# Kernel tuning notes

Measured on AMD Instinct MI355X. Metric: run time of the kernel, lower is better.

## Reference

```python
import jax, jax.numpy as jnp
import numpy as np

B, C, E, L = 128, 128, 10, 16  # atoms, channels, elements, num_ell (lmax=3)
K3_0, K2_0, K1_0 = 23, 4, 1    # num_params per correlation order, 0e output
K3_1, K2_1, K1_1 = 33, 6, 1    # num_params per correlation order, 1o output (num_equiv=3)


def setup_inputs() -> dict:
    key = jax.random.key(0)
    ks = jax.random.split(key, 16)
    inp = {
        'x': jax.random.normal(ks[0], (B, C, L), jnp.float32),
        'y': jax.random.uniform(ks[1], (B, E), jnp.float32),
        # generalized CG (U) buffers -- random dense stand-ins with faithful shapes
        'U1_0e': jax.random.normal(ks[2], (L, K1_0), jnp.float32),
        'U2_0e': jax.random.normal(ks[3], (L, L, K2_0), jnp.float32),
        'U3_0e': jax.random.normal(ks[4], (L, L, L, K3_0), jnp.float32),
        'U1_1o': jax.random.normal(ks[5], (3, L, K1_1), jnp.float32),
        'U2_1o': jax.random.normal(ks[6], (3, L, L, K2_1), jnp.float32),
        'U3_1o': jax.random.normal(ks[7], (3, L, L, L, K3_1), jnp.float32),
        # per-element weights, init randn/num_params as in torch
        'w1_0e': jax.random.normal(ks[8], (E, K1_0, C), jnp.float32) / K1_0,
        'w2_0e': jax.random.normal(ks[9], (E, K2_0, C), jnp.float32) / K2_0,
        'w3_0e': jax.random.normal(ks[10], (E, K3_0, C), jnp.float32) / K3_0,
        'w1_1o': jax.random.normal(ks[11], (E, K1_1, C), jnp.float32) / K1_1,
        'w2_1o': jax.random.normal(ks[12], (E, K2_1, C), jnp.float32) / K2_1,
        'w3_1o': jax.random.normal(ks[13], (E, K3_1, C), jnp.float32) / K3_1,
    }
    return inp


def _contract_0e(x, y, U1, U2, U3, w1, w2, w3):
    # main: 'wxik,ekc,bci,be->bcwx' (explicit path to control peak memory)
    wy3 = jnp.einsum('ekc,be->bkc', w3, y)              # [B,K3,C]
    t = jnp.einsum('wxik,bkc->bcwxi', U3, wy3)          # [B,C,L,L,L]
    out = jnp.einsum('bcwxi,bci->bcwx', t, x)           # [B,C,L,L]
    # order 2: weighting 'wxk,ekc,be->bcwx', features 'bcwi,bci->bcw'
    c2 = jnp.einsum('wxk,ekc,be->bcwx', U2, w2, y)
    out = jnp.einsum('bcwi,bci->bcw', c2 + out, x)
    # order 1: weighting 'wk,ekc,be->bcw', features 'bci,bci->bc'
    c1 = jnp.einsum('wk,ekc,be->bcw', U1, w1, y)
    out = jnp.einsum('bci,bci->bc', c1 + out, x)
    return out  # [B, C]


def _contract_1o(x, y, U1, U2, U3, w1, w2, w3):
    # main: 'wxvik,ekc,bci,be->bcwxv'  (w = equivariance dim of size 3)
    wy3 = jnp.einsum('ekc,be->bkc', w3, y)              # [B,K3,C]
    t = jnp.einsum('wxvik,bkc->bcwxvi', U3, wy3)        # [B,C,3,L,L,L]
    out = jnp.einsum('bcwxvi,bci->bcwxv', t, x)         # [B,C,3,L,L]
    # order 2: 'wxvk,ekc,be->bcwxv' ; features 'bcwxi,bci->bcwx'
    c2 = jnp.einsum('wxvk,ekc,be->bcwxv', U2, w2, y)
    out = jnp.einsum('bcwxi,bci->bcwx', c2 + out, x)
    # order 1: 'wxk,ekc,be->bcwx' ; features 'bcwi,bci->bcw'
    c1 = jnp.einsum('wxk,ekc,be->bcwx', U1, w1, y)
    out = jnp.einsum('bcwi,bci->bcw', c1 + out, x)
    return out.reshape(out.shape[0], -1)  # [B, 3*C]


def reference(x, y, U1_0e, U2_0e, U3_0e, U1_1o, U2_1o, U3_1o,
              w1_0e, w2_0e, w3_0e, w1_1o, w2_1o, w3_1o):
    out0 = _contract_0e(x, y, U1_0e, U2_0e, U3_0e, w1_0e, w2_0e, w3_0e)
    out1 = _contract_1o(x, y, U1_1o, U2_1o, U3_1o, w1_1o, w2_1o, w3_1o)
    return jnp.concatenate([out0, out1], axis=-1)  # [B, C + 3*C]
```

## Files before the change

### kernel.cpp

```cpp
#include <hip/hip_runtime.h>


typedef float  f32x4  __attribute__((ext_vector_type(4)));
typedef short  short8 __attribute__((ext_vector_type(8)));

namespace {
constexpr int EE  = 10;
constexpr int B1W = 552;
constexpr int B0W = 392;
constexpr int Z31 = 0;
constexpr int Z21 = 33;
constexpr int Z11 = 39;
constexpr int Z30 = 40;
constexpr int Z20 = 63;
constexpr int Z10 = 67;
constexpr int NZ  = 68;
}

__device__ __forceinline__ unsigned cvtpk(float lo, float hi) {
  unsigned r;
  asm("v_cvt_pk_bf16_f32 %0, %1, %2" : "=v"(r) : "v"(lo), "v"(hi));
  return r;
}

__device__ __forceinline__ short8 pack8(float f0, float f1, float f2, float f3,
                                        float f4, float f5, float f6, float f7) {
  union { short8 s; unsigned u[4]; } r;
  r.u[0] = cvtpk(f0, f1);
  r.u[1] = cvtpk(f2, f3);
  r.u[2] = cvtpk(f4, f5);
  r.u[3] = cvtpk(f6, f7);
  return r.s;
}

__global__ __launch_bounds__(512, 2) void symcon_mfma(
    const float* __restrict__ x,
    const float* __restrict__ y,
    const float* __restrict__ U1_0e,
    const float* __restrict__ U2_0e,
    const float* __restrict__ U3_0e,
    const float* __restrict__ U1_1o,
    const float* __restrict__ U2_1o,
    const float* __restrict__ U3_1o,
    const float* __restrict__ w1_0e, const float* __restrict__ w2_0e,
    const float* __restrict__ w3_0e, const float* __restrict__ w1_1o,
    const float* __restrict__ w2_1o, const float* __restrict__ w3_1o,
    float* __restrict__ out)
{
  __shared__ float x_lds[16][64];
  __shared__ float zbuf[NZ][64];
  __shared__ unsigned short B1buf[64][B1W];
  __shared__ unsigned short B0buf[64][B0W];
  __shared__ float red[8][64];

  const int tid   = threadIdx.x;
  const int blk   = blockIdx.x;
  const int pair0 = blk * 64;
  const int b     = blk >> 1;

  for (int t = tid; t < 16 * 64; t += 512) {
    const int i = t >> 6, n = t & 63;
    x_lds[i][n] = x[(size_t)(pair0 + n) * 16 + i];
  }
  for (int t = tid; t < NZ * 64; t += 512) {
    const int n  = t & 63;
    const int zi = t >> 6;
    const int c  = ((blk & 1) << 6) + n;
    const float* yb = y + b * EE;
    const float* wsrc; int stride;
    if      (zi < Z21) { wsrc = w3_1o + (zi      ) * 128 + c; stride = 33 * 128; }
    else if (zi < Z11) { wsrc = w2_1o + (zi - Z21) * 128 + c; stride =  6 * 128; }
    else if (zi < Z30) { wsrc = w1_1o +                    c; stride =  1 * 128; }
    else if (zi < Z20) { wsrc = w3_0e + (zi - Z30) * 128 + c; stride = 23 * 128; }
    else if (zi < Z10) { wsrc = w2_0e + (zi - Z20) * 128 + c; stride =  4 * 128; }
    else               { wsrc = w1_0e +                    c; stride =  1 * 128; }
    float a = 0.f;
    #pragma unroll
    for (int e = 0; e < EE; ++e) a += wsrc[e * stride] * yb[e];
    zbuf[zi][n] = a;
  }
  __syncthreads();

  auto b1valf = [&](int kap, int p) -> float {
    if (kap < 528) { int i = kap / 33, kk = kap - i * 33; return x_lds[i][p] * zbuf[Z31 + kk][p]; }
    if (kap < 534) return zbuf[Z21 + (kap - 528)][p];
    return 0.f;
  };
  auto b0valf = [&](int kap, int p) -> float {
    if (kap < 368) { int i = kap / 23, kk = kap - i * 23; return x_lds[i][p] * zbuf[Z30 + kk][p]; }
    if (kap < 372) return zbuf[Z20 + (kap - 368)][p];
    return 0.f;
  };
  #pragma unroll 1
  for (int idx = tid; idx < 272 * 64; idx += 512) {
    const int p = idx & 63, cp = idx >> 6;
    const int k0 = cp * 2;
    *(unsigned*)&B1buf[p][k0] = cvtpk(b1valf(k0, p), b1valf(k0 + 1, p));
  }
  #pragma unroll 1
  for (int idx = tid; idx < 192 * 64; idx += 512) {
    const int p = idx & 63, cp = idx >> 6;
    const int k0 = cp * 2;
    *(unsigned*)&B0buf[p][k0] = cvtpk(b0valf(k0, p), b0valf(k0 + 1, p));
  }
  __syncthreads();

  const int lane  = tid & 63;
  const int wv    = tid >> 6;
  const bool is1o = (wv < 6);
  const int q00   = (wv & 1) * 128;
  const int mbase = (is1o ? wv : (wv - 6)) * 128;
  const int lrow  = lane & 15;
  const int lgr   = lane >> 4;

  f32x4 acc[8][4] = {};

  if (is1o) {
    const float* __restrict__ U3r[8];
    #pragma unroll
    for (int mf = 0; mf < 8; ++mf)
      U3r[mf] = U3_1o + (size_t)(mbase + mf * 16 + lrow) * 528 + lgr * 8;
    #pragma unroll 2
    for (int t = 0; t < 16; ++t) {
      short8 af[8];
      #pragma unroll
      for (int mf = 0; mf < 8; ++mf) {
        f32x4 a  = *(const f32x4*)(U3r[mf] + t * 32);
        f32x4 bq = *(const f32x4*)(U3r[mf] + t * 32 + 4);
        af[mf] = pack8(a[0], a[1], a[2], a[3], bq[0], bq[1], bq[2], bq[3]);
      }
      short8 bfr[4];
      #pragma unroll
      for (int nf = 0; nf < 4; ++nf)
        bfr[nf] = *(const short8*)&B1buf[nf * 16 + lrow][t * 32 + lgr * 8];
      #pragma unroll
      for (int mf = 0; mf < 8; ++mf)
        #pragma unroll
        for (int nf = 0; nf < 4; ++nf)
          acc[mf][nf] = __builtin_amdgcn_mfma_f32_16x16x32_bf16(af[mf], bfr[nf], acc[mf][nf], 0, 0, 0);
    }
    {
      short8 af[8];
      #pragma unroll
      for (int mf = 0; mf < 8; ++mf) {
        const int row = mbase + mf * 16 + lrow;
        if (lgr < 2) {
          const float* p = U3_1o + (size_t)row * 528 + 512 + lgr * 8;
          f32x4 a = *(const f32x4*)p; f32x4 bq = *(const f32x4*)(p + 4);
          af[mf] = pack8(a[0], a[1], a[2], a[3], bq[0], bq[1], bq[2], bq[3]);
        } else if (lgr == 2) {
          const float* p = U2_1o + row * 6;
          af[mf] = pack8(p[0], p[1], p[2], p[3], p[4], p[5], 0.f, 0.f);
        } else {
          af[mf] = short8{0, 0, 0, 0, 0, 0, 0, 0};
        }
      }
      short8 bfr[4];
      #pragma unroll
      for (int nf = 0; nf < 4; ++nf)
        bfr[nf] = *(const short8*)&B1buf[nf * 16 + lrow][512 + lgr * 8];
      #pragma unroll
      for (int mf = 0; mf < 8; ++mf)
        #pragma unroll
        for (int nf = 0; nf < 4; ++nf)
          acc[mf][nf] = __builtin_amdgcn_mfma_f32_16x16x32_bf16(af[mf], bfr[nf], acc[mf][nf], 0, 0, 0);
    }
  } else {
    const float* __restrict__ U3r[8];
    #pragma unroll
    for (int mf = 0; mf < 8; ++mf)
      U3r[mf] = U3_0e + (size_t)(mbase + mf * 16 + lrow) * 368 + lgr * 8;
    #pragma unroll 2
    for (int t = 0; t < 11; ++t) {
      short8 af[8];
      #pragma unroll
      for (int mf = 0; mf < 8; ++mf) {
        f32x4 a  = *(const f32x4*)(U3r[mf] + t * 32);
        f32x4 bq = *(const f32x4*)(U3r[mf] + t * 32 + 4);
        af[mf] = pack8(a[0], a[1], a[2], a[3], bq[0], bq[1], bq[2], bq[3]);
      }
      short8 bfr[4];
      #pragma unroll
      for (int nf = 0; nf < 4; ++nf)
        bfr[nf] = *(const short8*)&B0buf[nf * 16 + lrow][t * 32 + lgr * 8];
      #pragma unroll
      for (int mf = 0; mf < 8; ++mf)
        #pragma unroll
        for (int nf = 0; nf < 4; ++nf)
          acc[mf][nf] = __builtin_amdgcn_mfma_f32_16x16x32_bf16(af[mf], bfr[nf], acc[mf][nf], 0, 0, 0);
    }
    {
      short8 af[8];
      #pragma unroll
      for (int mf = 0; mf < 8; ++mf) {
        const int row = mbase + mf * 16 + lrow;
        if (lgr < 2) {
          const float* p = U3_0e + (size_t)row * 368 + 352 + lgr * 8;
          f32x4 a = *(const f32x4*)p; f32x4 bq = *(const f32x4*)(p + 4);
          af[mf] = pack8(a[0], a[1], a[2], a[3], bq[0], bq[1], bq[2], bq[3]);
        } else if (lgr == 2) {
          const float* p = U2_0e + row * 4;
          af[mf] = pack8(p[0], p[1], p[2], p[3], 0.f, 0.f, 0.f, 0.f);
        } else {
          af[mf] = short8{0, 0, 0, 0, 0, 0, 0, 0};
        }
      }
      short8 bfr[4];
      #pragma unroll
      for (int nf = 0; nf < 4; ++nf)
        bfr[nf] = *(const short8*)&B0buf[nf * 16 + lrow][352 + lgr * 8];
      #pragma unroll
      for (int mf = 0; mf < 8; ++mf)
        #pragma unroll
        for (int nf = 0; nf < 4; ++nf)
          acc[mf][nf] = __builtin_amdgcn_mfma_f32_16x16x32_bf16(af[mf], bfr[nf], acc[mf][nf], 0, 0, 0);
    }
  }

  float s[4] = {0.f, 0.f, 0.f, 0.f};
  const int rg = lgr * 4;
  #pragma unroll
  for (int mf = 0; mf < 8; ++mf) {
    #pragma unroll
    for (int reg = 0; reg < 4; ++reg) {
      const int q  = q00 + mf * 16 + rg + reg;
      const int qa = q >> 4, qb = q & 15;
      #pragma unroll
      for (int nf = 0; nf < 4; ++nf) {
        const int p = nf * 16 + lrow;
        s[nf] += acc[mf][nf][reg] * (x_lds[qa][p] * x_lds[qb][p]);
      }
    }
  }
  #pragma unroll
  for (int nf = 0; nf < 4; ++nf) {
    s[nf] += __shfl_xor(s[nf], 16);
    s[nf] += __shfl_xor(s[nf], 32);
  }
  if (lane < 16) {
    #pragma unroll
    for (int nf = 0; nf < 4; ++nf) red[wv][nf * 16 + lane] = s[nf];
  }
  __syncthreads();

  if (tid < 256) {
    const int slot = tid >> 6;
    const int n    = tid & 63;
    const int cc   = ((blk & 1) << 6) + n;
    if (slot < 3) {
      float u1 = 0.f;
      #pragma unroll
      for (int xx = 0; xx < 16; ++xx) u1 += U1_1o[slot * 16 + xx] * x_lds[xx][n];
      out[(size_t)b * 512 + 128 + cc * 3 + slot] =
          red[2 * slot][n] + red[2 * slot + 1][n] + zbuf[Z11][n] * u1;
    } else {
      float u1 = 0.f;
      #pragma unroll
      for (int xx = 0; xx < 16; ++xx) u1 += U1_0e[xx] * x_lds[xx][n];
      out[(size_t)b * 512 + cc] =
          red[6][n] + red[7][n] + zbuf[Z10][n] * u1;
    }
  }
}

extern "C" void kernel_launch(void* const* d_in, const int* in_sizes, int n_in,
                              void* d_out, int out_size, void* d_ws, size_t ws_size,
                              hipStream_t stream) {
  const float* x     = (const float*)d_in[0];
  const float* y     = (const float*)d_in[1];
  const float* U1_0e = (const float*)d_in[2];
  const float* U2_0e = (const float*)d_in[3];
  const float* U3_0e = (const float*)d_in[4];
  const float* U1_1o = (const float*)d_in[5];
  const float* U2_1o = (const float*)d_in[6];
  const float* U3_1o = (const float*)d_in[7];
  const float* w1_0e = (const float*)d_in[8];
  const float* w2_0e = (const float*)d_in[9];
  const float* w3_0e = (const float*)d_in[10];
  const float* w1_1o = (const float*)d_in[11];
  const float* w2_1o = (const float*)d_in[12];
  const float* w3_1o = (const float*)d_in[13];
  (void)in_sizes; (void)n_in; (void)out_size; (void)d_ws; (void)ws_size;

  hipLaunchKernelGGL(symcon_mfma, dim3(256), dim3(512), 0, stream,
                     x, y, U1_0e, U2_0e, U3_0e, U1_1o, U2_1o, U3_1o,
                     w1_0e, w2_0e, w3_0e, w1_1o, w2_1o, w3_1o,
                     (float*)d_out);
}
```

Baseline: 54.94 us.

## Split 1o and 0e paths into separate blocks with smaller per-wave tiles

Each block previously handled both the 1o and 0e contractions for a 64-pair tile with 8 waves. The kernel now launches twice as many blocks of 12 waves. The first half computes only the 1o output, using 4 M-fragments per wave, and the second half computes only 0e, with 8 active waves of 2 fragments each. Shared memory is a union of the two layouts, which shrinks LDS per block. The intent is more parallelism, lower register pressure and better occupancy, at the cost of unbalanced block work and idle waves in the 0e blocks.

```diff
diff --git a/kernel.cpp b/kernel.cpp
--- a/kernel.cpp
+++ b/kernel.cpp
@@ -5,16 +5,21 @@
 typedef short  short8 __attribute__((ext_vector_type(8)));
 
 namespace {
-constexpr int EE  = 10;
-constexpr int B1W = 552;
-constexpr int B0W = 392;
-constexpr int Z31 = 0;
-constexpr int Z21 = 33;
-constexpr int Z11 = 39;
-constexpr int Z30 = 40;
-constexpr int Z20 = 63;
-constexpr int Z10 = 67;
-constexpr int NZ  = 68;
+constexpr int EE = 10;
+
+struct Sh1 {
+  unsigned short B1[64][552];
+  float x[16][64];
+  float z[40][64];
+  float red[12][64];
+};
+struct Sh0 {
+  unsigned short B0[64][392];
+  float x[16][64];
+  float z[28][64];
+  float red[8][64];
+};
+union ShU { Sh1 o1; Sh0 o0; };
 }
 
 __device__ __forceinline__ unsigned cvtpk(float lo, float hi) {
@@ -33,7 +38,7 @@
   return r.s;
 }
 
-__global__ __launch_bounds__(512, 2) void symcon_mfma(
+__global__ __launch_bounds__(768) void symcon_mfma(
     const float* __restrict__ x,
     const float* __restrict__ y,
     const float* __restrict__ U1_0e,
@@ -47,84 +52,74 @@
     const float* __restrict__ w2_1o, const float* __restrict__ w3_1o,
     float* __restrict__ out)
 {
-  __shared__ float x_lds[16][64];
-  __shared__ float zbuf[NZ][64];
-  __shared__ unsigned short B1buf[64][B1W];
-  __shared__ unsigned short B0buf[64][B0W];
-  __shared__ float red[8][64];
+  __shared__ ShU sh;
 
   const int tid   = threadIdx.x;
   const int blk   = blockIdx.x;
-  const int pair0 = blk * 64;
-  const int b     = blk >> 1;
-
-  for (int t = tid; t < 16 * 64; t += 512) {
-    const int i = t >> 6, n = t & 63;
-    x_lds[i][n] = x[(size_t)(pair0 + n) * 16 + i];
-  }
-  for (int t = tid; t < NZ * 64; t += 512) {
-    const int n  = t & 63;
-    const int zi = t >> 6;
-    const int c  = ((blk & 1) << 6) + n;
-    const float* yb = y + b * EE;
-    const float* wsrc; int stride;
-    if      (zi < Z21) { wsrc = w3_1o + (zi      ) * 128 + c; stride = 33 * 128; }
-    else if (zi < Z11) { wsrc = w2_1o + (zi - Z21) * 128 + c; stride =  6 * 128; }
-    else if (zi < Z30) { wsrc = w1_1o +                    c; stride =  1 * 128; }
-    else if (zi < Z20) { wsrc = w3_0e + (zi - Z30) * 128 + c; stride = 23 * 128; }
-    else if (zi < Z10) { wsrc = w2_0e + (zi - Z20) * 128 + c; stride =  4 * 128; }
-    else               { wsrc = w1_0e +                    c; stride =  1 * 128; }
-    float a = 0.f;
-    #pragma unroll
-    for (int e = 0; e < EE; ++e) a += wsrc[e * stride] * yb[e];
-    zbuf[zi][n] = a;
-  }
-  __syncthreads();
-
-  auto b1valf = [&](int kap, int p) -> float {
-    if (kap < 528) { int i = kap / 33, kk = kap - i * 33; return x_lds[i][p] * zbuf[Z31 + kk][p]; }
-    if (kap < 534) return zbuf[Z21 + (kap - 528)][p];
-    return 0.f;
-  };
-  auto b0valf = [&](int kap, int p) -> float {
-    if (kap < 368) { int i = kap / 23, kk = kap - i * 23; return x_lds[i][p] * zbuf[Z30 + kk][p]; }
-    if (kap < 372) return zbuf[Z20 + (kap - 368)][p];
-    return 0.f;
-  };
-  #pragma unroll 1
-  for (int idx = tid; idx < 272 * 64; idx += 512) {
-    const int p = idx & 63, cp = idx >> 6;
-    const int k0 = cp * 2;
-    *(unsigned*)&B1buf[p][k0] = cvtpk(b1valf(k0, p), b1valf(k0 + 1, p));
-  }
-  #pragma unroll 1
-  for (int idx = tid; idx < 192 * 64; idx += 512) {
-    const int p = idx & 63, cp = idx >> 6;
-    const int k0 = cp * 2;
-    *(unsigned*)&B0buf[p][k0] = cvtpk(b0valf(k0, p), b0valf(k0 + 1, p));
-  }
-  __syncthreads();
-
+  const bool is1o = (blk < 256);
+  const int pblk  = is1o ? blk : blk - 256;
+  const int pair0 = pblk * 64;
+  const int b     = pblk >> 1;
   const int lane  = tid & 63;
   const int wv    = tid >> 6;
-  const bool is1o = (wv < 6);
-  const int q00   = (wv & 1) * 128;
-  const int mbase = (is1o ? wv : (wv - 6)) * 128;
   const int lrow  = lane & 15;
   const int lgr   = lane >> 4;
 
-  f32x4 acc[8][4] = {};
-
   if (is1o) {
-    const float* __restrict__ U3r[8];
+    for (int t = tid; t < 16 * 64; t += 768) {
+      const int i = t >> 6, n = t & 63;
+      sh.o1.x[i][n] = x[(size_t)(pair0 + n) * 16 + i];
+    }
+    for (int t = tid; t < 40 * 64; t += 768) {
+      const int n  = t & 63;
+      const int zi = t >> 6;
+      const int c  = ((pblk & 1) << 6) + n;
+      const float* yb = y + b * EE;
+      const float* wsrc; int stride;
+      if      (zi < 33) { wsrc = w3_1o + zi * 128 + c;        stride = 33 * 128; }
+      else if (zi < 39) { wsrc = w2_1o + (zi - 33) * 128 + c; stride =  6 * 128; }
+      else              { wsrc = w1_1o + c;                   stride =      128; }
+      float a = 0.f;
+      #pragma unroll
+      for (int e = 0; e < EE; ++e) a += wsrc[e * stride] * yb[e];
+      sh.o1.z[zi][n] = a;
+    }
+    __syncthreads();
+
+    #pragma unroll 1
+    for (int idx = tid; idx < 272 * 64; idx += 768) {
+      const int p = idx & 63, cp = idx >> 6;
+      const int k0 = cp * 2;
+      float v0, v1;
+      if (k0 < 528) {
+        const int i = k0 / 33, kk = k0 - i * 33;
+        v0 = sh.o1.x[i][p] * sh.o1.z[kk][p];
+        const int k1 = k0 + 1;
+        const int i1 = k1 / 33, kk1 = k1 - i1 * 33;
+        v1 = sh.o1.x[i1][p] * sh.o1.z[kk1][p];
+      } else if (k0 < 534) {
+        v0 = sh.o1.z[33 + (k0 - 528)][p];
+        v1 = (k0 + 1 < 534) ? sh.o1.z[33 + (k0 - 527)][p] : 0.f;
+      } else {
+        v0 = 0.f; v1 = 0.f;
+      }
+      *(unsigned*)&sh.o1.B1[p][k0] = cvtpk(v0, v1);
+    }
+    __syncthreads();
+
+    const int mbase = wv * 64;
+    const float* __restrict__ U3r[4];
     #pragma unroll
-    for (int mf = 0; mf < 8; ++mf)
+    for (int mf = 0; mf < 4; ++mf)
       U3r[mf] = U3_1o + (size_t)(mbase + mf * 16 + lrow) * 528 + lgr * 8;
+
+    f32x4 acc[4][4] = {};
+
     #pragma unroll 2
     for (int t = 0; t < 16; ++t) {
-      short8 af[8];
-      #pragma unroll
-      for (int mf = 0; mf < 8; ++mf) {
+      short8 af[4];
+      #pragma unroll
+      for (int mf = 0; mf < 4; ++mf) {
         f32x4 a  = *(const f32x4*)(U3r[mf] + t * 32);
         f32x4 bq = *(const f32x4*)(U3r[mf] + t * 32 + 4);
         af[mf] = pack8(a[0], a[1], a[2], a[3], bq[0], bq[1], bq[2], bq[3]);
@@ -132,17 +127,17 @@
       short8 bfr[4];
       #pragma unroll
       for (int nf = 0; nf < 4; ++nf)
-        bfr[nf] = *(const short8*)&B1buf[nf * 16 + lrow][t * 32 + lgr * 8];
-      #pragma unroll
-      for (int mf = 0; mf < 8; ++mf)
+        bfr[nf] = *(const short8*)&sh.o1.B1[nf * 16 + lrow][t * 32 + lgr * 8];
+      #pragma unroll
+      for (int mf = 0; mf < 4; ++mf)
         #pragma unroll
         for (int nf = 0; nf < 4; ++nf)
           acc[mf][nf] = __builtin_amdgcn_mfma_f32_16x16x32_bf16(af[mf], bfr[nf], acc[mf][nf], 0, 0, 0);
     }
     {
-      short8 af[8];
-      #pragma unroll
-      for (int mf = 0; mf < 8; ++mf) {
+      short8 af[4];
+      #pragma unroll
+      for (int mf = 0; mf < 4; ++mf) {
         const int row = mbase + mf * 16 + lrow;
         if (lgr < 2) {
           const float* p = U3_1o + (size_t)row * 528 + 512 + lgr * 8;
@@ -158,107 +153,185 @@
       short8 bfr[4];
       #pragma unroll
       for (int nf = 0; nf < 4; ++nf)
-        bfr[nf] = *(const short8*)&B1buf[nf * 16 + lrow][512 + lgr * 8];
-      #pragma unroll
-      for (int mf = 0; mf < 8; ++mf)
+        bfr[nf] = *(const short8*)&sh.o1.B1[nf * 16 + lrow][512 + lgr * 8];
+      #pragma unroll
+      for (int mf = 0; mf < 4; ++mf)
         #pragma unroll
         for (int nf = 0; nf < 4; ++nf)
           acc[mf][nf] = __builtin_amdgcn_mfma_f32_16x16x32_bf16(af[mf], bfr[nf], acc[mf][nf], 0, 0, 0);
     }
+
+    float s[4] = {0.f, 0.f, 0.f, 0.f};
+    const int rg = lgr * 4;
+    #pragma unroll
+    for (int mf = 0; mf < 4; ++mf) {
+      #pragma unroll
+      for (int reg = 0; reg < 4; ++reg) {
+        const int q  = (mbase + mf * 16 + rg + reg) & 255;
+        const int qa = q >> 4, qb = q & 15;
+        #pragma unroll
+        for (int nf = 0; nf < 4; ++nf) {
+          const int p = nf * 16 + lrow;
+          s[nf] += acc[mf][nf][reg] * (sh.o1.x[qa][p] * sh.o1.x[qb][p]);
+        }
+      }
+    }
+    #pragma unroll
+    for (int nf = 0; nf < 4; ++nf) {
+      s[nf] += __shfl_xor(s[nf], 16);
+      s[nf] += __shfl_xor(s[nf], 32);
+    }
+    if (lane < 16) {
+      #pragma unroll
+      for (int nf = 0; nf < 4; ++nf) sh.o1.red[wv][nf * 16 + lane] = s[nf];
+    }
+    __syncthreads();
+
+    if (tid < 192) {
+      const int slot = tid >> 6;
+      const int n    = tid & 63;
+      const int cc   = ((pblk & 1) << 6) + n;
+      float v = sh.o1.red[4 * slot][n] + sh.o1.red[4 * slot + 1][n]
+              + sh.o1.red[4 * slot + 2][n] + sh.o1.red[4 * slot + 3][n];
+      float u1 = 0.f;
+      #pragma unroll
+      for (int xx = 0; xx < 16; ++xx) u1 += U1_1o[slot * 16 + xx] * sh.o1.x[xx][n];
+      out[(size_t)b * 512 + 128 + cc * 3 + slot] = v + sh.o1.z[39][n] * u1;
+    }
   } else {
-    const float* __restrict__ U3r[8];
-    #pragma unroll
-    for (int mf = 0; mf < 8; ++mf)
-      U3r[mf] = U3_0e + (size_t)(mbase + mf * 16 + lrow) * 368 + lgr * 8;
-    #pragma unroll 2
-    for (int t = 0; t < 11; ++t) {
-      short8 af[8];
-      #pragma unroll
-      for (int mf = 0; mf < 8; ++mf) {
-        f32x4 a  = *(const f32x4*)(U3r[mf] + t * 32);
-        f32x4 bq = *(const f32x4*)(U3r[mf] + t * 32 + 4);
-        af[mf] = pack8(a[0], a[1], a[2], a[3], bq[0], bq[1], bq[2], bq[3]);
-      }
-      short8 bfr[4];
-      #pragma unroll
-      for (int nf = 0; nf < 4; ++nf)
-        bfr[nf] = *(const short8*)&B0buf[nf * 16 + lrow][t * 32 + lgr * 8];
-      #pragma unroll
-      for (int mf = 0; mf < 8; ++mf)
+    for (int t = tid; t < 16 * 64; t += 768) {
+      const int i = t >> 6, n = t & 63;
+      sh.o0.x[i][n] = x[(size_t)(pair0 + n) * 16 + i];
+    }
+    for (int t = tid; t < 28 * 64; t += 768) {
+      const int n  = t & 63;
+      const int zi = t >> 6;
+      const int c  = ((pblk & 1) << 6) + n;
+      const float* yb = y + b * EE;
+      const float* wsrc; int stride;
+      if      (zi < 23) { wsrc = w3_0e + zi * 128 + c;        stride = 23 * 128; }
+      else if (zi < 27) { wsrc = w2_0e + (zi - 23) * 128 + c; stride =  4 * 128; }
+      else              { wsrc = w1_0e + c;                   stride =      128; }
+      float a = 0.f;
+      #pragma unroll
+      for (int e = 0; e < EE; ++e) a += wsrc[e * stride] * yb[e];
+      sh.o0.z[zi][n] = a;
+    }
+    __syncthreads();
+
+    #pragma unroll 1
+    for (int idx = tid; idx < 192 * 64; idx += 768) {
+      const int p = idx & 63, cp = idx >> 6;
+      const int k0 = cp * 2;
+      float v0, v1;
+      if (k0 < 368) {
+        const int i = k0 / 23, kk = k0 - i * 23;
+        v0 = sh.o0.x[i][p] * sh.o0.z[kk][p];
+        const int k1 = k0 + 1;
+        const int i1 = k1 / 23, kk1 = k1 - i1 * 23;
+        v1 = sh.o0.x[i1][p] * sh.o0.z[kk1][p];
+      } else if (k0 < 372) {
+        v0 = sh.o0.z[23 + (k0 - 368)][p];
+        v1 = (k0 + 1 < 372) ? sh.o0.z[23 + (k0 - 367)][p] : 0.f;
+      } else {
+        v0 = 0.f; v1 = 0.f;
+      }
+      *(unsigned*)&sh.o0.B0[p][k0] = cvtpk(v0, v1);
+    }
+    __syncthreads();
+
+    if (wv < 8) {
+      const int mbase = wv * 32;
+      const float* __restrict__ U3r[2];
+      #pragma unroll
+      for (int mf = 0; mf < 2; ++mf)
+        U3r[mf] = U3_0e + (size_t)(mbase + mf * 16 + lrow) * 368 + lgr * 8;
+
+      f32x4 acc[2][4] = {};
+
+      #pragma unroll 2
+      for (int t = 0; t < 11; ++t) {
+        short8 af[2];
+        #pragma unroll
+        for (int mf = 0; mf < 2; ++mf) {
+          f32x4 a  = *(const f32x4*)(U3r[mf] + t * 32);
+          f32x4 bq = *(const f32x4*)(U3r[mf] + t * 32 + 4);
+          af[mf] = pack8(a[0], a[1], a[2], a[3], bq[0], bq[1], bq[2], bq[3]);
+        }
+        short8 bfr[4];
         #pragma unroll
         for (int nf = 0; nf < 4; ++nf)
-          acc[mf][nf] = __builtin_amdgcn_mfma_f32_16x16x32_bf16(af[mf], bfr[nf], acc[mf][nf], 0, 0, 0);
-    }
-    {
-      short8 af[8];
-      #pragma unroll
-      for (int mf = 0; mf < 8; ++mf) {
-        const int row = mbase + mf * 16 + lrow;
-        if (lgr < 2) {
-          const float* p = U3_0e + (size_t)row * 368 + 352 + lgr * 8;
-          f32x4 a = *(const f32x4*)p; f32x4 bq = *(const f32x4*)(p + 4);
-          af[mf] = pack8(a[0], a[1], a[2], a[3], bq[0], bq[1], bq[2], bq[3]);
-        } else if (lgr == 2) {
-          const float* p = U2_0e + row * 4;
-          af[mf] = pack8(p[0], p[1], p[2], p[3], 0.f, 0.f, 0.f, 0.f);
-        } else {
-          af[mf] = short8{0, 0, 0, 0, 0, 0, 0, 0};
-        }
-      }
-      short8 bfr[4];
-      #pragma unroll
-      for (int nf = 0; nf < 4; ++nf)
-        bfr[nf] = *(const short8*)&B0buf[nf * 16 + lrow][352 + lgr * 8];
-      #pragma unroll
-      for (int mf = 0; mf < 8; ++mf)
+          bfr[nf] = *(const short8*)&sh.o0.B0[nf * 16 + lrow][t * 32 + lgr * 8];
+        #pragma unroll
+        for (int mf = 0; mf < 2; ++mf)
+          #pragma unroll
+          for (int nf = 0; nf < 4; ++nf)
+            acc[mf][nf] = __builtin_amdgcn_mfma_f32_16x16x32_bf16(af[mf], bfr[nf], acc[mf][nf], 0, 0, 0);
+      }
+      {
+        short8 af[2];
+        #pragma unroll
+        for (int mf = 0; mf < 2; ++mf) {
+          const int row = mbase + mf * 16 + lrow;
+          if (lgr < 2) {
+            const float* p = U3_0e + (size_t)row * 368 + 352 + lgr * 8;
+            f32x4 a = *(const f32x4*)p; f32x4 bq = *(const f32x4*)(p + 4);
+            af[mf] = pack8(a[0], a[1], a[2], a[3], bq[0], bq[1], bq[2], bq[3]);
+          } else if (lgr == 2) {
+            const float* p = U2_0e + row * 4;
+            af[mf] = pack8(p[0], p[1], p[2], p[3], 0.f, 0.f, 0.f, 0.f);
+          } else {
+            af[mf] = short8{0, 0, 0, 0, 0, 0, 0, 0};
+          }
+        }
+        short8 bfr[4];
         #pragma unroll
         for (int nf = 0; nf < 4; ++nf)
-          acc[mf][nf] = __builtin_amdgcn_mfma_f32_16x16x32_bf16(af[mf], bfr[nf], acc[mf][nf], 0, 0, 0);
-    }
-  }
-
-  float s[4] = {0.f, 0.f, 0.f, 0.f};
-  const int rg = lgr * 4;
-  #pragma unroll
-  for (int mf = 0; mf < 8; ++mf) {
-    #pragma unroll
-    for (int reg = 0; reg < 4; ++reg) {
-      const int q  = q00 + mf * 16 + rg + reg;
-      const int qa = q >> 4, qb = q & 15;
+          bfr[nf] = *(const short8*)&sh.o0.B0[nf * 16 + lrow][352 + lgr * 8];
+        #pragma unroll
+        for (int mf = 0; mf < 2; ++mf)
+          #pragma unroll
+          for (int nf = 0; nf < 4; ++nf)
+            acc[mf][nf] = __builtin_amdgcn_mfma_f32_16x16x32_bf16(af[mf], bfr[nf], acc[mf][nf], 0, 0, 0);
+      }
+
+      float s[4] = {0.f, 0.f, 0.f, 0.f};
+      const int rg = lgr * 4;
+      #pragma unroll
+      for (int mf = 0; mf < 2; ++mf) {
+        #pragma unroll
+        for (int reg = 0; reg < 4; ++reg) {
+          const int q  = mbase + mf * 16 + rg + reg;
+          const int qa = q >> 4, qb = q & 15;
+          #pragma unroll
+          for (int nf = 0; nf < 4; ++nf) {
+            const int p = nf * 16 + lrow;
+            s[nf] += acc[mf][nf][reg] * (sh.o0.x[qa][p] * sh.o0.x[qb][p]);
+          }
+        }
+      }
       #pragma unroll
       for (int nf = 0; nf < 4; ++nf) {
-        const int p = nf * 16 + lrow;
-        s[nf] += acc[mf][nf][reg] * (x_lds[qa][p] * x_lds[qb][p]);
-      }
-    }
-  }
-  #pragma unroll
-  for (int nf = 0; nf < 4; ++nf) {
-    s[nf] += __shfl_xor(s[nf], 16);
-    s[nf] += __shfl_xor(s[nf], 32);
-  }
-  if (lane < 16) {
-    #pragma unroll
-    for (int nf = 0; nf < 4; ++nf) red[wv][nf * 16 + lane] = s[nf];
-  }
-  __syncthreads();
-
-  if (tid < 256) {
-    const int slot = tid >> 6;
-    const int n    = tid & 63;
-    const int cc   = ((blk & 1) << 6) + n;
-    if (slot < 3) {
+        s[nf] += __shfl_xor(s[nf], 16);
+        s[nf] += __shfl_xor(s[nf], 32);
+      }
+      if (lane < 16) {
+        #pragma unroll
+        for (int nf = 0; nf < 4; ++nf) sh.o0.red[wv][nf * 16 + lane] = s[nf];
+      }
+    }
+    __syncthreads();
+
+    if (tid < 64) {
+      const int n  = tid;
+      const int cc = ((pblk & 1) << 6) + n;
+      float v = 0.f;
+      #pragma unroll
+      for (int k = 0; k < 8; ++k) v += sh.o0.red[k][n];
       float u1 = 0.f;
       #pragma unroll
-      for (int xx = 0; xx < 16; ++xx) u1 += U1_1o[slot * 16 + xx] * x_lds[xx][n];
-      out[(size_t)b * 512 + 128 + cc * 3 + slot] =
-          red[2 * slot][n] + red[2 * slot + 1][n] + zbuf[Z11][n] * u1;
-    } else {
-      float u1 = 0.f;
-      #pragma unroll
-      for (int xx = 0; xx < 16; ++xx) u1 += U1_0e[xx] * x_lds[xx][n];
-      out[(size_t)b * 512 + cc] =
-          red[6][n] + red[7][n] + zbuf[Z10][n] * u1;
+      for (int xx = 0; xx < 16; ++xx) u1 += U1_0e[xx] * sh.o0.x[xx][n];
+      out[(size_t)b * 512 + cc] = v + sh.o0.z[27][n] * u1;
     }
   }
 }
@@ -282,7 +355,7 @@
   const float* w3_1o = (const float*)d_in[13];
   (void)in_sizes; (void)n_in; (void)out_size; (void)d_ws; (void)ws_size;
 
-  hipLaunchKernelGGL(symcon_mfma, dim3(256), dim3(512), 0, stream,
+  hipLaunchKernelGGL(symcon_mfma, dim3(512), dim3(768), 0, stream,
                      x, y, U1_0e, U2_0e, U3_0e, U1_1o, U2_1o, U3_1o,
                      w1_0e, w2_0e, w3_0e, w1_1o, w2_1o, w3_1o,
                      (float*)d_out);
```

Result: slower. 56.37 us (+2.6%).
